# Optimization experiments

Measured on AMD Instinct MI355X. Metric: run time of the kernel, lower is better.

## Reference

```python
import jax, jax.numpy as jnp
import numpy as np

B, T, I, O, M = 64, 512, 256, 1024, 8
MS = O // M          # module_size
IM = I * M           # input_dim * num_modules


def setup_inputs() -> dict:
    key = jax.random.key(0)
    ks = jax.random.split(key, 6)
    s = 0.02
    return {
        "x": jax.random.normal(ks[0], (B, T, I), dtype=jnp.float32),
        "W_in": jax.random.normal(ks[1], (O, I), dtype=jnp.float32) * s,
        "b_in": jnp.zeros((O,), dtype=jnp.float32),
        "W_h": jax.random.normal(ks[2], (O, O), dtype=jnp.float32) * s,
        "W_ir": jax.random.normal(ks[3], (IM, I), dtype=jnp.float32) * s,
        "b_ir": jnp.zeros((IM,), dtype=jnp.float32),
        "W_hr": jax.random.normal(ks[4], (IM, IM), dtype=jnp.float32) * s,
        "module_periods": jnp.ones((M,), dtype=jnp.float32),
        "module_shifts": jnp.zeros((M,), dtype=jnp.float32),
    }


def reference(x, W_in, b_in, W_h, W_ir, b_ir, W_hr, module_periods, module_shifts):
    # x: [B, T, I]
    def step(carry, inp):
        h, x_pred = carry           # h: [B,O], x_pred: [B,IM]
        ti, xi = inp                # ti scalar float, xi: [B,I]
        acts = jnp.tanh(xi @ W_in.T + b_in + h @ W_h.T)            # [B,O]
        acts_rec = jnp.tanh(xi @ W_ir.T + b_ir + x_pred @ W_hr.T)  # [B,IM]
        m_xp = x_pred.reshape(B, M, I)
        # NOTE: nn.LogSoftmax() with no dim on a 3D tensor defaults to dim=0 (batch axis)
        surprisal = jax.nn.log_softmax(m_xp, axis=0) * xi[:, None, :]  # [B,M,I]
        mean_surprisal = surprisal.mean(-1)                            # [B,M]
        mp = mean_surprisal * module_periods                           # [B,M]
        gate = (jnp.sin(ti * mp + module_shifts) + 1.0) * 0.5          # [B,M]
        gate_full = jnp.repeat(gate, MS, axis=-1)                      # [B,O]
        y = (1.0 - gate_full) * acts + gate_full * h
        return (y, acts_rec), (y, mp)

    ts = jnp.arange(T, dtype=x.dtype)
    carry0 = (jnp.zeros((B, O), dtype=x.dtype), jnp.zeros((B, IM), dtype=x.dtype))
    (h_final, _), (ys, ps) = jax.lax.scan(step, carry0, (ts, jnp.swapaxes(x, 0, 1)))
    ys = jnp.swapaxes(ys, 0, 1)   # [B,T,O]
    ps = jnp.swapaxes(ps, 0, 1)   # [B,T,M]
    return ys, h_final, ps
```

## Files before the change

kernel.cpp:

```cpp
#include <hip/hip_runtime.h>
#include <hip/hip_fp16.h>

typedef _Float16 f16;
typedef f16 f16x8 __attribute__((ext_vector_type(8)));
typedef f16 f16x4 __attribute__((ext_vector_type(4)));
typedef float f32x4 __attribute__((ext_vector_type(4)));
typedef float f32x16 __attribute__((ext_vector_type(16)));

#define B_ 64
#define T_ 512
#define I_ 256
#define O_ 1024
#define M_ 8
#define IM_ 2048
#define NREC 64
#define NB 96
#define THREADS 256

#define OFF_X16 4096ull
#define SZ_X16  ((unsigned long long)T_ * B_ * I_ * 2)
#define OFF_XP3 (OFF_X16 + SZ_X16)
#define SZ_XP3  (3ull * B_ * IM_ * 2)
#define OFF_H2  (OFF_XP3 + SZ_XP3)

#define BAR_LEAF(i) ((i) * 16)
#define BAR_CENT    128
#define BAR_REPL(i) (192 + (i) * 16)

#define WAITV(N) asm volatile("s_waitcnt vmcnt(" #N ")" ::: "memory")
#define LGKM0    asm volatile("s_waitcnt lgkmcnt(0)" ::: "memory")
#define SCHEDB   __builtin_amdgcn_sched_barrier(0)
#define BARRIER  __builtin_amdgcn_s_barrier()

#define ISSUE_AX(BUF, P) asm volatile( \
    "global_load_dwordx4 %0, %8, off\n\t" \
    "global_load_dwordx4 %1, %8, off offset:32\n\t" \
    "global_load_dwordx4 %2, %8, off offset:64\n\t" \
    "global_load_dwordx4 %3, %8, off offset:96\n\t" \
    "global_load_dwordx4 %4, %8, off offset:128\n\t" \
    "global_load_dwordx4 %5, %8, off offset:160\n\t" \
    "global_load_dwordx4 %6, %8, off offset:192\n\t" \
    "global_load_dwordx4 %7, %8, off offset:224" \
    : "=&v"(abuf[BUF][0]), "=&v"(abuf[BUF][1]), "=&v"(abuf[BUF][2]), "=&v"(abuf[BUF][3]), \
      "=&v"(abuf[BUF][4]), "=&v"(abuf[BUF][5]), "=&v"(abuf[BUF][6]), "=&v"(abuf[BUF][7]) \
    : "v"(P) : "memory")

#define ISSUE_AS(BUF, P) asm volatile( \
    "global_load_dwordx4 %0, %8, off sc0 sc1\n\t" \
    "global_load_dwordx4 %1, %8, off offset:32 sc0 sc1\n\t" \
    "global_load_dwordx4 %2, %8, off offset:64 sc0 sc1\n\t" \
    "global_load_dwordx4 %3, %8, off offset:96 sc0 sc1\n\t" \
    "global_load_dwordx4 %4, %8, off offset:128 sc0 sc1\n\t" \
    "global_load_dwordx4 %5, %8, off offset:160 sc0 sc1\n\t" \
    "global_load_dwordx4 %6, %8, off offset:192 sc0 sc1\n\t" \
    "global_load_dwordx4 %7, %8, off offset:224 sc0 sc1" \
    : "=&v"(abuf[BUF][0]), "=&v"(abuf[BUF][1]), "=&v"(abuf[BUF][2]), "=&v"(abuf[BUF][3]), \
      "=&v"(abuf[BUF][4]), "=&v"(abuf[BUF][5]), "=&v"(abuf[BUF][6]), "=&v"(abuf[BUF][7]) \
    : "v"(P) : "memory")

#define ISSUE_STG8(P0,P1,P2,P3,P4,P5,P6,P7) asm volatile( \
    "global_load_dwordx4 %0, %8, off sc0 sc1\n\t" \
    "global_load_dwordx4 %1, %9, off sc0 sc1\n\t" \
    "global_load_dwordx4 %2, %10, off sc0 sc1\n\t" \
    "global_load_dwordx4 %3, %11, off sc0 sc1\n\t" \
    "global_load_dwordx4 %4, %12, off sc0 sc1\n\t" \
    "global_load_dwordx4 %5, %13, off sc0 sc1\n\t" \
    "global_load_dwordx4 %6, %14, off sc0 sc1\n\t" \
    "global_load_dwordx4 %7, %15, off sc0 sc1" \
    : "=&v"(sreg[0]), "=&v"(sreg[1]), "=&v"(sreg[2]), "=&v"(sreg[3]), \
      "=&v"(sreg[4]), "=&v"(sreg[5]), "=&v"(sreg[6]), "=&v"(sreg[7]) \
    : "v"(P0), "v"(P1), "v"(P2), "v"(P3), "v"(P4), "v"(P5), "v"(P6), "v"(P7) \
    : "memory")

#define GM_PRO(J) do { \
    const int c_ = c0 + (J); \
    if (c_ < 2) { const char* p_ = xrow + c_ * 256;  ISSUE_AX(J, p_); } \
    else        { const char* p_ = sprow + c_ * 256; ISSUE_AS(J, p_); } \
} while (0)

#define GM_ITR(I, WN, DOISS) do { \
    WAITV(WN); \
    _Pragma("unroll") \
    for (int kb = 0; kb < 8; ++kb) { \
        f16x8 bf = *(const f16x8*)(smem + addrB[kb] + (I) * 256); \
        if (kb & 1) acc1 = __builtin_amdgcn_mfma_f32_32x32x16_f16(abuf[(I) & 3][kb], bf, acc1, 0, 0, 0); \
        else        acc0 = __builtin_amdgcn_mfma_f32_32x32x16_f16(abuf[(I) & 3][kb], bf, acc0, 0, 0, 0); \
    } \
    SCHEDB; \
    if (DOISS) { const char* p_ = sprow + (c0 + (I) + 4) * 256; ISSUE_AS(((I) & 3), p_); } \
} while (0)

#define GM_ITA(I, WN, DOISS) do { \
    WAITV(WN); \
    _Pragma("unroll") \
    for (int kb = 0; kb < 8; ++kb) { \
        f16x8 bf = *(const f16x8*)(smem + addrB[kb] + (I) * 256); \
        if (kb & 1) acc1 = __builtin_amdgcn_mfma_f32_32x32x16_f16(abuf[(I) % 3][kb], bf, acc1, 0, 0, 0); \
        else        acc0 = __builtin_amdgcn_mfma_f32_32x32x16_f16(abuf[(I) % 3][kb], bf, acc0, 0, 0, 0); \
    } \
    SCHEDB; \
    if (DOISS) { const char* p_ = sprow + (c0 + (I) + 3) * 256; ISSUE_AS(((I) % 3), p_); } \
} while (0)

__device__ __forceinline__ void st_coh_h(f16* p, float vf) {
    union { f16 h; short s; } u; u.h = (f16)vf;
    asm volatile("global_store_short %0, %1, off sc0 sc1" :: "v"(p), "v"((int)u.s) : "memory");
}

__device__ __forceinline__ float fast_tanh(float x) {
    float e = __expf(2.f * x);
    return 1.f - 2.f / (e + 1.f);
}

__device__ __forceinline__ unsigned ld_rlx(unsigned* p) {
    return __hip_atomic_load(p, __ATOMIC_RELAXED, __HIP_MEMORY_SCOPE_AGENT);
}

__device__ __forceinline__ void arrive_all(unsigned* bar, int blk, int t) {
    unsigned old = __hip_atomic_fetch_add(&bar[BAR_LEAF(blk & 7)], 1u, __ATOMIC_RELAXED, __HIP_MEMORY_SCOPE_AGENT);
    if (old % 12u == 11u) {
        unsigned r = __hip_atomic_fetch_add(&bar[BAR_CENT], 1u, __ATOMIC_RELAXED, __HIP_MEMORY_SCOPE_AGENT);
        if ((r & 7u) == 7u) {
            unsigned v = (unsigned)(t + 1);
            #pragma unroll
            for (int i = 0; i < 8; ++i) {
                unsigned* rp = &bar[BAR_REPL(i)];
                asm volatile("global_store_dword %0, %1, off sc0 sc1" :: "v"(rp), "v"(v) : "memory");
            }
        }
    }
}

__global__ void init_kernel(const float* __restrict__ x, char* __restrict__ ws) {
    const int gid = blockIdx.x * THREADS + threadIdx.x;
    if (blockIdx.x == 0) {
        for (int i = threadIdx.x; i < 512; i += THREADS) ((unsigned*)ws)[i] = 0u;
    }
    f16* x16 = (f16*)(ws + OFF_X16);
    const int NQ = T_ * B_ * (I_ / 4);
    for (int q = gid; q < NQ; q += 256 * THREADS) {
        int t = q >> 12;
        int rem = q & 4095;
        int b = rem >> 6;
        int k4 = rem & 63;
        f32x4 v = *(const f32x4*)(x + ((size_t)b * T_ + t) * I_ + k4 * 4);
        f16x4 h;
        h[0] = (f16)v[0]; h[1] = (f16)v[1]; h[2] = (f16)v[2]; h[3] = (f16)v[3];
        *(f16x4*)(x16 + ((size_t)t * B_ + b) * I_ + k4 * 4) = h;
    }
    f16x8 z = {0, 0, 0, 0, 0, 0, 0, 0};
    f16* xp0 = (f16*)(ws + OFF_XP3);
    for (int e = gid * 8; e < B_ * IM_; e += 256 * THREADS * 8) *(f16x8*)(xp0 + e) = z;
    f16* h0 = (f16*)(ws + OFF_H2);
    for (int e = gid * 8; e < B_ * O_; e += 256 * THREADS * 8) *(f16x8*)(h0 + e) = z;
}

__global__ __launch_bounds__(THREADS, 1) void cwrnn_kernel(
    const float* __restrict__ x, const float* __restrict__ W_in, const float* __restrict__ b_in,
    const float* __restrict__ W_h, const float* __restrict__ W_ir, const float* __restrict__ b_ir,
    const float* __restrict__ W_hr, const float* __restrict__ periods, const float* __restrict__ shifts,
    float* __restrict__ out, char* __restrict__ ws)
{
    __shared__ __align__(16) char smem[157696];

    unsigned* bar = (unsigned*)ws;
    const int blk = blockIdx.x, tid = threadIdx.x;
    const int lane = tid & 63, w = tid >> 6;
    const int col = lane & 31, g = lane >> 5;
    const int pair = w >> 1;
    const int arow = ((w & 1) << 5) + col;

    float* ys = out;
    float* hfin = out + (size_t)B_ * T_ * O_;
    float* ps = hfin + (size_t)B_ * O_;

    unsigned* myrepl = &bar[BAR_REPL(blk & 7)];

    if (blk < NREC) {
        const int j0 = blk * 32;
        {
            const int j = tid >> 3;
            const float* ra = W_ir + (size_t)(j0 + j) * I_;
            const float* rb = W_hr + (size_t)(j0 + j) * IM_ - 256;
            for (int u = (tid & 7); u < 288; u += 8) {
                int k0 = u * 8;
                const float* s = (k0 < 256) ? (ra + k0) : (rb + k0);
                f32x4 lo = *(const f32x4*)s;
                f32x4 hi = *(const f32x4*)(s + 4);
                f16x8 v;
                #pragma unroll
                for (int e = 0; e < 4; ++e) { v[e] = (f16)lo[e]; v[e + 4] = (f16)hi[e]; }
                *(f16x8*)(smem + j * 4608 + ((u ^ (j & 15)) << 4)) = v;
            }
        }
        const float bir = b_ir[j0 + col];
        LGKM0; BARRIER;

        int addrB[8];
        const int c0 = pair * 9;
        #pragma unroll
        for (int kb = 0; kb < 8; ++kb)
            addrB[kb] = col * 4608 + ((((kb << 1) + g) ^ (col & 15)) << 4) + c0 * 256;

        const char* xrow0 = (const char*)(ws + OFF_X16) + (size_t)arow * 512 + g * 16;
        f16* const xpB = (f16*)(ws + OFF_XP3);

        for (int t = 0; t < T_ - 1; ++t) {
            if (tid == 0) {
                while ((int)ld_rlx(myrepl) < t) __builtin_amdgcn_s_sleep(2);
            }
            BARRIER;
            const int bi = t % 3;
            int bn = bi + 1; if (bn == 3) bn = 0;
            const f16* xpcur = xpB + (size_t)bi * B_ * IM_;
            f16* xpnxt = xpB + (size_t)bn * B_ * IM_;
            const char* sprow = (const char*)xpcur + (size_t)arow * 4096 + g * 16 - 512;
            const char* xrow = xrow0 + (size_t)t * 32768;

            f16x8 abuf[4][8];
            f32x16 acc0, acc1;
            #pragma unroll
            for (int r = 0; r < 16; ++r) { acc0[r] = 0.f; acc1[r] = 0.f; }

            GM_PRO(0); GM_PRO(1); GM_PRO(2); GM_PRO(3);
            GM_ITR(0, 24, 1); GM_ITR(1, 24, 1); GM_ITR(2, 24, 1); GM_ITR(3, 24, 1);
            GM_ITR(4, 24, 1); GM_ITR(5, 24, 0); GM_ITR(6, 16, 0); GM_ITR(7, 8, 0); GM_ITR(8, 0, 0);

            f32x16 accS;
            #pragma unroll
            for (int r = 0; r < 16; ++r) accS[r] = acc0[r] + acc1[r];
            if (w >= 2) {
                char* axp = smem + 147456 + (w - 2) * 5120 + lane * 80;
                #pragma unroll
                for (int q = 0; q < 4; ++q) {
                    f32x4 v = { accS[q * 4 + 0], accS[q * 4 + 1], accS[q * 4 + 2], accS[q * 4 + 3] };
                    *(f32x4*)(axp + q * 16) = v;
                }
            }
            LGKM0; BARRIER;
            if (w < 2) {
                const char* axp = smem + 147456 + w * 5120 + lane * 80;
                #pragma unroll
                for (int q = 0; q < 4; ++q) {
                    f32x4 v = *(const f32x4*)(axp + q * 16);
                    accS[q * 4 + 0] += v[0]; accS[q * 4 + 1] += v[1];
                    accS[q * 4 + 2] += v[2]; accS[q * 4 + 3] += v[3];
                }
                #pragma unroll
                for (int r = 0; r < 16; ++r) {
                    int row = (r & 3) + ((r >> 2) << 3) + (g << 2) + (w << 5);
                    st_coh_h(xpnxt + (size_t)row * IM_ + j0 + col, fast_tanh(accS[r] + bir));
                }
            }
            WAITV(0);
            BARRIER;
            if (tid == 0) arrive_all(bar, blk, t);
        }
    } else {
        const int a = blk - NREC;
        const int m = a >> 2;
        const int o0 = a * 32;
        {
            const int j = tid >> 3;
            const float* ra = W_in + (size_t)(o0 + j) * I_;
            const float* rb = W_h + (size_t)(o0 + j) * O_ - 256;
            for (int u = (tid & 7); u < 160; u += 8) {
                int k0 = u * 8;
                const float* s = (k0 < 256) ? (ra + k0) : (rb + k0);
                f32x4 lo = *(const f32x4*)s;
                f32x4 hi = *(const f32x4*)(s + 4);
                f16x8 v;
                #pragma unroll
                for (int e = 0; e < 4; ++e) { v[e] = (f16)lo[e]; v[e + 4] = (f16)hi[e]; }
                *(f16x8*)(smem + j * 2560 + ((u ^ (j & 15)) << 4)) = v;
            }
        }
        const float bin = b_in[o0 + col];
        const float per = periods[m], shf = shifts[m];
        LGKM0; BARRIER;

        int addrB[8];
        const int c0 = pair * 5;
        #pragma unroll
        for (int kb = 0; kb < 8; ++kb)
            addrB[kb] = col * 2560 + ((((kb << 1) + g) ^ (col & 15)) << 4) + c0 * 256;

        char* xp_raw = smem + 81920;
        float* lse_lds = (float*)(smem + 124928);
        float* part_lds = (float*)(smem + 125952);
        float* gate_lds = (float*)(smem + 126976);

        const char* xrow0 = (const char*)(ws + OFF_X16) + (size_t)arow * 512 + g * 16;
        const f16* xpB = (const f16*)(ws + OFF_XP3);
        f16* h2 = (f16*)(ws + OFF_H2);
        const int t5 = tid >> 5, cg = tid & 31;
        float hreg[16];
        #pragma unroll
        for (int r = 0; r < 16; ++r) hreg[r] = 0.f;

        for (int t = 0; t < T_; ++t) {
            if (tid == 0) {
                while ((int)ld_rlx(myrepl) < t) __builtin_amdgcn_s_sleep(2);
            }
            BARRIER;
            const int bi = t % 3;
            const f16* xpcur = xpB + (size_t)bi * B_ * IM_;
            const f16* hcur = h2 + (size_t)(t & 1) * B_ * O_;
            f16* hnxt = h2 + (size_t)((t + 1) & 1) * B_ * O_;

            f16x8 sreg[8];
            {
                const char* sb = (const char*)xpcur + (size_t)m * 512 + (size_t)cg * 16 + (size_t)t5 * 4096;
                ISSUE_STG8(sb, sb + 32768, sb + 2 * 32768, sb + 3 * 32768,
                           sb + 4 * 32768, sb + 5 * 32768, sb + 6 * 32768, sb + 7 * 32768);
            }

            const char* sprow = (const char*)hcur + (size_t)arow * 2048 + g * 16 - 512;
            const char* xrow = xrow0 + (size_t)t * 32768;
            f16x8 abuf[3][8];
            f32x16 acc0, acc1;
            #pragma unroll
            for (int r = 0; r < 16; ++r) { acc0[r] = 0.f; acc1[r] = 0.f; }

            GM_PRO(0); GM_PRO(1); GM_PRO(2);
            WAITV(16);
            {
                const int gsw = (cg ^ t5) << 4;
                #pragma unroll
                for (int k = 0; k < 8; ++k)
                    *(f16x8*)(xp_raw + (size_t)(t5 + (k << 3)) * 512 + gsw) = sreg[k];
            }
            #pragma unroll
            for (int kb = 0; kb < 8; ++kb) {
                f16x8 bf = *(const f16x8*)(smem + addrB[kb]);
                if (kb & 1) acc1 = __builtin_amdgcn_mfma_f32_32x32x16_f16(abuf[0][kb], bf, acc1, 0, 0, 0);
                else        acc0 = __builtin_amdgcn_mfma_f32_32x32x16_f16(abuf[0][kb], bf, acc0, 0, 0, 0);
            }
            SCHEDB;
            { const char* p_ = sprow + (c0 + 3) * 256; ISSUE_AS(0, p_); }
            GM_ITA(1, 16, 1); GM_ITA(2, 16, 0); GM_ITA(3, 8, 0); GM_ITA(4, 0, 0);

            f32x16 accS;
            #pragma unroll
            for (int r = 0; r < 16; ++r) accS[r] = acc0[r] + acc1[r];
            if (w >= 2) {
                char* axp = smem + 114688 + (w - 2) * 5120 + lane * 80;
                #pragma unroll
                for (int q = 0; q < 4; ++q) {
                    f32x4 v = { accS[q * 4 + 0], accS[q * 4 + 1], accS[q * 4 + 2], accS[q * 4 + 3] };
                    *(f32x4*)(axp + q * 16) = v;
                }
            }
            LGKM0; BARRIER;
            {
                int i = tid;
                int gq = i >> 3, r2 = (i & 7) * 2;
                float s = 0.f;
                #pragma unroll 8
                for (int b = 0; b < B_; ++b)
                    s += __expf((float)*(const f16*)(xp_raw + b * 512 + ((gq ^ (b & 7)) << 4) + r2));
                lse_lds[i] = __logf(s);
            }
            LGKM0; BARRIER;
            {
                int b = tid >> 2, q = tid & 3;
                const float* xr = x + ((size_t)b * T_ + t) * I_ + q * 64;
                float s = 0.f;
                #pragma unroll
                for (int k = 0; k < 8; ++k) {
                    f16x8 xp8 = *(const f16x8*)(xp_raw + (size_t)b * 512 + ((((q << 3) + k) ^ (b & 7)) << 4));
                    f32x4 xa = *(const f32x4*)(xr + k * 8);
                    f32x4 xb2 = *(const f32x4*)(xr + k * 8 + 4);
                    #pragma unroll
                    for (int jj = 0; jj < 4; ++jj)
                        s += ((float)xp8[jj] - lse_lds[(q << 6) + (k << 3) + jj]) * xa[jj];
                    #pragma unroll
                    for (int jj = 0; jj < 4; ++jj)
                        s += ((float)xp8[jj + 4] - lse_lds[(q << 6) + (k << 3) + 4 + jj]) * xb2[jj];
                }
                part_lds[tid] = s;
            }
            LGKM0; BARRIER;
            if (tid < B_) {
                float s = part_lds[tid * 4] + part_lds[tid * 4 + 1] + part_lds[tid * 4 + 2] + part_lds[tid * 4 + 3];
                float mp = (s * (1.f / 256.f)) * per;
                gate_lds[tid] = 0.5f * (sinf((float)t * mp + shf) + 1.f);
                if ((a & 3) == 0) ps[((size_t)tid * T_ + t) * M_ + m] = mp;
            }
            LGKM0; BARRIER;
            if (w < 2) {
                const char* axp = smem + 114688 + w * 5120 + lane * 80;
                #pragma unroll
                for (int q = 0; q < 4; ++q) {
                    f32x4 v = *(const f32x4*)(axp + q * 16);
                    accS[q * 4 + 0] += v[0]; accS[q * 4 + 1] += v[1];
                    accS[q * 4 + 2] += v[2]; accS[q * 4 + 3] += v[3];
                }
                #pragma unroll
                for (int r = 0; r < 16; ++r) {
                    int row = (r & 3) + ((r >> 2) << 3) + (g << 2) + (w << 5);
                    float gt = gate_lds[row];
                    float av = fast_tanh(accS[r] + bin);
                    float y = (1.f - gt) * av + gt * hreg[r];
                    hreg[r] = y;
                    st_coh_h(hnxt + (size_t)row * O_ + o0 + col, y);
                    ys[((size_t)row * T_ + t) * O_ + o0 + col] = y;
                    if (t == T_ - 1) hfin[(size_t)row * O_ + o0 + col] = y;
                }
            }
            WAITV(0);
            BARRIER;
            if (tid == 0) arrive_all(bar, blk, t);
        }
    }
}

extern "C" void kernel_launch(void* const* d_in, const int* in_sizes, int n_in,
                              void* d_out, int out_size, void* d_ws, size_t ws_size,
                              hipStream_t stream) {
    const float* x    = (const float*)d_in[0];
    const float* W_in = (const float*)d_in[1];
    const float* b_in = (const float*)d_in[2];
    const float* W_h  = (const float*)d_in[3];
    const float* W_ir = (const float*)d_in[4];
    const float* b_ir = (const float*)d_in[5];
    const float* W_hr = (const float*)d_in[6];
    const float* per  = (const float*)d_in[7];
    const float* shf  = (const float*)d_in[8];

    hipLaunchKernelGGL(init_kernel, dim3(256), dim3(THREADS), 0, stream,
                       x, (char*)d_ws);
    hipLaunchKernelGGL(cwrnn_kernel, dim3(NB), dim3(THREADS), 0, stream,
                       x, W_in, b_in, W_h, W_ir, b_ir, W_hr, per, shf,
                       (float*)d_out, (char*)d_ws);
}
```

Before: 6.467 ms.

## Split grid barrier into two groups and widen blocks to six waves

```diff
diff --git a/kernel.cpp b/kernel.cpp
--- a/kernel.cpp
+++ b/kernel.cpp
@@ -15,7 +15,7 @@
 #define IM_ 2048
 #define NREC 64
 #define NB 96
-#define THREADS 256
+#define THREADS 384
 
 #define OFF_X16 4096ull
 #define SZ_X16  ((unsigned long long)T_ * B_ * I_ * 2)
@@ -23,9 +23,20 @@
 #define SZ_XP3  (3ull * B_ * IM_ * 2)
 #define OFF_H2  (OFF_XP3 + SZ_XP3)
 
-#define BAR_LEAF(i) ((i) * 16)
-#define BAR_CENT    128
-#define BAR_REPL(i) (192 + (i) * 16)
+#define LEAFA(i) ((i) * 16)
+#define CENTA    128
+#define FLAGA(i) (192 + (i) * 16)
+#define LEAFB(i) (320 + (i) * 16)
+#define CENTB    448
+#define FLAGB(i) (512 + (i) * 16)
+
+#define CMB_REC 147456
+#define CMB_ACT 114688
+#define XPRAW   81920
+#define LSE_O   122880
+#define PART_O  123904
+#define GATE_O  124928
+#define SMEM_SZ 155648
 
 #define WAITV(N) asm volatile("s_waitcnt vmcnt(" #N ")" ::: "memory")
 #define LGKM0    asm volatile("s_waitcnt lgkmcnt(0)" ::: "memory")
@@ -58,7 +69,7 @@
       "=&v"(abuf[BUF][4]), "=&v"(abuf[BUF][5]), "=&v"(abuf[BUF][6]), "=&v"(abuf[BUF][7]) \
     : "v"(P) : "memory")
 
-#define ISSUE_STG8(P0,P1,P2,P3,P4,P5,P6,P7) asm volatile( \
+#define ISSUE_STGA(ARR, P0,P1,P2,P3,P4,P5,P6,P7) asm volatile( \
     "global_load_dwordx4 %0, %8, off sc0 sc1\n\t" \
     "global_load_dwordx4 %1, %9, off sc0 sc1\n\t" \
     "global_load_dwordx4 %2, %10, off sc0 sc1\n\t" \
@@ -67,30 +78,18 @@
     "global_load_dwordx4 %5, %13, off sc0 sc1\n\t" \
     "global_load_dwordx4 %6, %14, off sc0 sc1\n\t" \
     "global_load_dwordx4 %7, %15, off sc0 sc1" \
-    : "=&v"(sreg[0]), "=&v"(sreg[1]), "=&v"(sreg[2]), "=&v"(sreg[3]), \
-      "=&v"(sreg[4]), "=&v"(sreg[5]), "=&v"(sreg[6]), "=&v"(sreg[7]) \
+    : "=&v"((ARR)[0]), "=&v"((ARR)[1]), "=&v"((ARR)[2]), "=&v"((ARR)[3]), \
+      "=&v"((ARR)[4]), "=&v"((ARR)[5]), "=&v"((ARR)[6]), "=&v"((ARR)[7]) \
     : "v"(P0), "v"(P1), "v"(P2), "v"(P3), "v"(P4), "v"(P5), "v"(P6), "v"(P7) \
     : "memory")
 
 #define GM_PRO(J) do { \
-    const int c_ = c0 + (J); \
+    const int c_ = c0k + (J); \
     if (c_ < 2) { const char* p_ = xrow + c_ * 256;  ISSUE_AX(J, p_); } \
     else        { const char* p_ = sprow + c_ * 256; ISSUE_AS(J, p_); } \
 } while (0)
 
-#define GM_ITR(I, WN, DOISS) do { \
-    WAITV(WN); \
-    _Pragma("unroll") \
-    for (int kb = 0; kb < 8; ++kb) { \
-        f16x8 bf = *(const f16x8*)(smem + addrB[kb] + (I) * 256); \
-        if (kb & 1) acc1 = __builtin_amdgcn_mfma_f32_32x32x16_f16(abuf[(I) & 3][kb], bf, acc1, 0, 0, 0); \
-        else        acc0 = __builtin_amdgcn_mfma_f32_32x32x16_f16(abuf[(I) & 3][kb], bf, acc0, 0, 0, 0); \
-    } \
-    SCHEDB; \
-    if (DOISS) { const char* p_ = sprow + (c0 + (I) + 4) * 256; ISSUE_AS(((I) & 3), p_); } \
-} while (0)
-
-#define GM_ITA(I, WN, DOISS) do { \
+#define GM_IT(I, WN, DOISS) do { \
     WAITV(WN); \
     _Pragma("unroll") \
     for (int kb = 0; kb < 8; ++kb) { \
@@ -99,7 +98,7 @@
         else        acc0 = __builtin_amdgcn_mfma_f32_32x32x16_f16(abuf[(I) % 3][kb], bf, acc0, 0, 0, 0); \
     } \
     SCHEDB; \
-    if (DOISS) { const char* p_ = sprow + (c0 + (I) + 3) * 256; ISSUE_AS(((I) % 3), p_); } \
+    if (DOISS) { const char* p_ = sprow + (c0k + (I) + 3) * 256; ISSUE_AS(((I) % 3), p_); } \
 } while (0)
 
 __device__ __forceinline__ void st_coh_h(f16* p, float vf) {
@@ -116,29 +115,37 @@
     return __hip_atomic_load(p, __ATOMIC_RELAXED, __HIP_MEMORY_SCOPE_AGENT);
 }
 
-__device__ __forceinline__ void arrive_all(unsigned* bar, int blk, int t) {
-    unsigned old = __hip_atomic_fetch_add(&bar[BAR_LEAF(blk & 7)], 1u, __ATOMIC_RELAXED, __HIP_MEMORY_SCOPE_AGENT);
-    if (old % 12u == 11u) {
-        unsigned r = __hip_atomic_fetch_add(&bar[BAR_CENT], 1u, __ATOMIC_RELAXED, __HIP_MEMORY_SCOPE_AGENT);
-        if ((r & 7u) == 7u) {
-            unsigned v = (unsigned)(t + 1);
-            #pragma unroll
-            for (int i = 0; i < 8; ++i) {
-                unsigned* rp = &bar[BAR_REPL(i)];
-                asm volatile("global_store_dword %0, %1, off sc0 sc1" :: "v"(rp), "v"(v) : "memory");
-            }
-        }
+__device__ __forceinline__ void post_flags(unsigned* bar, int base, unsigned v) {
+    #pragma unroll
+    for (int i = 0; i < 8; ++i) {
+        unsigned* rp = &bar[base + i * 16];
+        asm volatile("global_store_dword %0, %1, off sc0 sc1" :: "v"(rp), "v"(v) : "memory");
     }
 }
 
+__device__ __forceinline__ void arriveA(unsigned* bar, int blk, int t) {
+    unsigned old = __hip_atomic_fetch_add(&bar[LEAFA(blk & 7)], 1u, __ATOMIC_RELAXED, __HIP_MEMORY_SCOPE_AGENT);
+    if ((old & 7u) == 7u) {
+        unsigned r = __hip_atomic_fetch_add(&bar[CENTA], 1u, __ATOMIC_RELAXED, __HIP_MEMORY_SCOPE_AGENT);
+        if ((r & 7u) == 7u) post_flags(bar, FLAGA(0), (unsigned)(t + 1));
+    }
+}
+__device__ __forceinline__ void arriveB(unsigned* bar, int a, int t) {
+    unsigned old = __hip_atomic_fetch_add(&bar[LEAFB(a & 7)], 1u, __ATOMIC_RELAXED, __HIP_MEMORY_SCOPE_AGENT);
+    if ((old & 3u) == 3u) {
+        unsigned r = __hip_atomic_fetch_add(&bar[CENTB], 1u, __ATOMIC_RELAXED, __HIP_MEMORY_SCOPE_AGENT);
+        if ((r & 7u) == 7u) post_flags(bar, FLAGB(0), (unsigned)(t + 1));
+    }
+}
+
 __global__ void init_kernel(const float* __restrict__ x, char* __restrict__ ws) {
-    const int gid = blockIdx.x * THREADS + threadIdx.x;
+    const int gid = blockIdx.x * 256 + threadIdx.x;
     if (blockIdx.x == 0) {
-        for (int i = threadIdx.x; i < 512; i += THREADS) ((unsigned*)ws)[i] = 0u;
+        for (int i = threadIdx.x; i < 1024; i += 256) ((unsigned*)ws)[i] = 0u;
     }
     f16* x16 = (f16*)(ws + OFF_X16);
     const int NQ = T_ * B_ * (I_ / 4);
-    for (int q = gid; q < NQ; q += 256 * THREADS) {
+    for (int q = gid; q < NQ; q += 256 * 256) {
         int t = q >> 12;
         int rem = q & 4095;
         int b = rem >> 6;
@@ -150,9 +157,9 @@
     }
     f16x8 z = {0, 0, 0, 0, 0, 0, 0, 0};
     f16* xp0 = (f16*)(ws + OFF_XP3);
-    for (int e = gid * 8; e < B_ * IM_; e += 256 * THREADS * 8) *(f16x8*)(xp0 + e) = z;
+    for (int e = gid * 8; e < B_ * IM_; e += 256 * 256 * 8) *(f16x8*)(xp0 + e) = z;
     f16* h0 = (f16*)(ws + OFF_H2);
-    for (int e = gid * 8; e < B_ * O_; e += 256 * THREADS * 8) *(f16x8*)(h0 + e) = z;
+    for (int e = gid * 8; e < B_ * O_; e += 256 * 256 * 8) *(f16x8*)(h0 + e) = z;
 }
 
 __global__ __launch_bounds__(THREADS, 1) void cwrnn_kernel(
@@ -161,28 +168,27 @@
     const float* __restrict__ W_hr, const float* __restrict__ periods, const float* __restrict__ shifts,
     float* __restrict__ out, char* __restrict__ ws)
 {
-    __shared__ __align__(16) char smem[157696];
+    __shared__ __align__(16) char smem[SMEM_SZ];
 
     unsigned* bar = (unsigned*)ws;
     const int blk = blockIdx.x, tid = threadIdx.x;
     const int lane = tid & 63, w = tid >> 6;
     const int col = lane & 31, g = lane >> 5;
-    const int pair = w >> 1;
-    const int arow = ((w & 1) << 5) + col;
+    const int rg = w & 1;
+    const int kg = w >> 1;
+    const int arow = (rg << 5) + col;
 
     float* ys = out;
     float* hfin = out + (size_t)B_ * T_ * O_;
     float* ps = hfin + (size_t)B_ * O_;
 
-    unsigned* myrepl = &bar[BAR_REPL(blk & 7)];
-
     if (blk < NREC) {
         const int j0 = blk * 32;
         {
-            const int j = tid >> 3;
+            const int j = tid & 31;
             const float* ra = W_ir + (size_t)(j0 + j) * I_;
             const float* rb = W_hr + (size_t)(j0 + j) * IM_ - 256;
-            for (int u = (tid & 7); u < 288; u += 8) {
+            for (int u = (tid >> 5); u < 288; u += 12) {
                 int k0 = u * 8;
                 const float* s = (k0 < 256) ? (ra + k0) : (rb + k0);
                 f32x4 lo = *(const f32x4*)s;
@@ -197,17 +203,24 @@
         LGKM0; BARRIER;
 
         int addrB[8];
-        const int c0 = pair * 9;
+        const int c0k = kg * 6;
         #pragma unroll
         for (int kb = 0; kb < 8; ++kb)
-            addrB[kb] = col * 4608 + ((((kb << 1) + g) ^ (col & 15)) << 4) + c0 * 256;
+            addrB[kb] = col * 4608 + ((((kb << 1) + g) ^ (col & 15)) << 4) + c0k * 256;
 
         const char* xrow0 = (const char*)(ws + OFF_X16) + (size_t)arow * 512 + g * 16;
         f16* const xpB = (f16*)(ws + OFF_XP3);
+        unsigned* fA = &bar[FLAGA(blk & 7)];
+        unsigned* fB = &bar[FLAGB(blk & 7)];
 
         for (int t = 0; t < T_ - 1; ++t) {
             if (tid == 0) {
-                while ((int)ld_rlx(myrepl) < t) __builtin_amdgcn_s_sleep(2);
+                while (1) {
+                    int fa = (int)ld_rlx(fA);
+                    int fb = (int)ld_rlx(fB);
+                    if (fa >= t && fb >= t - 2) break;
+                    __builtin_amdgcn_s_sleep(2);
+                }
             }
             BARRIER;
             const int bi = t % 3;
@@ -217,54 +230,74 @@
             const char* sprow = (const char*)xpcur + (size_t)arow * 4096 + g * 16 - 512;
             const char* xrow = xrow0 + (size_t)t * 32768;
 
-            f16x8 abuf[4][8];
+            f16x8 abuf[3][8];
             f32x16 acc0, acc1;
             #pragma unroll
             for (int r = 0; r < 16; ++r) { acc0[r] = 0.f; acc1[r] = 0.f; }
 
-            GM_PRO(0); GM_PRO(1); GM_PRO(2); GM_PRO(3);
-            GM_ITR(0, 24, 1); GM_ITR(1, 24, 1); GM_ITR(2, 24, 1); GM_ITR(3, 24, 1);
-            GM_ITR(4, 24, 1); GM_ITR(5, 24, 0); GM_ITR(6, 16, 0); GM_ITR(7, 8, 0); GM_ITR(8, 0, 0);
+            GM_PRO(0); GM_PRO(1); GM_PRO(2);
+            GM_IT(0, 16, 1); GM_IT(1, 16, 1); GM_IT(2, 16, 1);
+            GM_IT(3, 16, 0); GM_IT(4, 8, 0); GM_IT(5, 0, 0);
 
             f32x16 accS;
             #pragma unroll
             for (int r = 0; r < 16; ++r) accS[r] = acc0[r] + acc1[r];
-            if (w >= 2) {
-                char* axp = smem + 147456 + (w - 2) * 5120 + lane * 80;
-                #pragma unroll
-                for (int q = 0; q < 4; ++q) {
-                    f32x4 v = { accS[q * 4 + 0], accS[q * 4 + 1], accS[q * 4 + 2], accS[q * 4 + 3] };
-                    *(f32x4*)(axp + q * 16) = v;
-                }
-            }
-            LGKM0; BARRIER;
-            if (w < 2) {
-                const char* axp = smem + 147456 + w * 5120 + lane * 80;
-                #pragma unroll
-                for (int q = 0; q < 4; ++q) {
-                    f32x4 v = *(const f32x4*)(axp + q * 16);
-                    accS[q * 4 + 0] += v[0]; accS[q * 4 + 1] += v[1];
-                    accS[q * 4 + 2] += v[2]; accS[q * 4 + 3] += v[3];
+
+            if (kg == 1) {
+                char* cb = smem + CMB_REC + rg * 4096 + lane * 16;
+                #pragma unroll
+                for (int q = 0; q < 4; ++q) {
+                    f32x4 v = { accS[q*4+0], accS[q*4+1], accS[q*4+2], accS[q*4+3] };
+                    *(f32x4*)(cb + q * 1024) = v;
+                }
+            }
+            LGKM0; BARRIER;
+            if (kg == 0) {
+                const char* cb = smem + CMB_REC + rg * 4096 + lane * 16;
+                #pragma unroll
+                for (int q = 0; q < 4; ++q) {
+                    f32x4 v = *(const f32x4*)(cb + q * 1024);
+                    accS[q*4+0] += v[0]; accS[q*4+1] += v[1];
+                    accS[q*4+2] += v[2]; accS[q*4+3] += v[3];
+                }
+            }
+            LGKM0; BARRIER;
+            if (kg == 2) {
+                char* cb = smem + CMB_REC + rg * 4096 + lane * 16;
+                #pragma unroll
+                for (int q = 0; q < 4; ++q) {
+                    f32x4 v = { accS[q*4+0], accS[q*4+1], accS[q*4+2], accS[q*4+3] };
+                    *(f32x4*)(cb + q * 1024) = v;
+                }
+            }
+            LGKM0; BARRIER;
+            if (kg == 0) {
+                const char* cb = smem + CMB_REC + rg * 4096 + lane * 16;
+                #pragma unroll
+                for (int q = 0; q < 4; ++q) {
+                    f32x4 v = *(const f32x4*)(cb + q * 1024);
+                    accS[q*4+0] += v[0]; accS[q*4+1] += v[1];
+                    accS[q*4+2] += v[2]; accS[q*4+3] += v[3];
                 }
                 #pragma unroll
                 for (int r = 0; r < 16; ++r) {
-                    int row = (r & 3) + ((r >> 2) << 3) + (g << 2) + (w << 5);
+                    int row = (r & 3) + ((r >> 2) << 3) + (g << 2) + (rg << 5);
                     st_coh_h(xpnxt + (size_t)row * IM_ + j0 + col, fast_tanh(accS[r] + bir));
                 }
             }
             WAITV(0);
             BARRIER;
-            if (tid == 0) arrive_all(bar, blk, t);
+            if (tid == 0) arriveA(bar, blk, t);
         }
     } else {
         const int a = blk - NREC;
         const int m = a >> 2;
         const int o0 = a * 32;
         {
-            const int j = tid >> 3;
+            const int j = tid & 31;
             const float* ra = W_in + (size_t)(o0 + j) * I_;
             const float* rb = W_h + (size_t)(o0 + j) * O_ - 256;
-            for (int u = (tid & 7); u < 160; u += 8) {
+            for (int u = (tid >> 5); u < 160; u += 12) {
                 int k0 = u * 8;
                 const float* s = (k0 < 256) ? (ra + k0) : (rb + k0);
                 f32x4 lo = *(const f32x4*)s;
@@ -280,27 +313,33 @@
         LGKM0; BARRIER;
 
         int addrB[8];
-        const int c0 = pair * 5;
+        const int c0k = kg * 4;
         #pragma unroll
         for (int kb = 0; kb < 8; ++kb)
-            addrB[kb] = col * 2560 + ((((kb << 1) + g) ^ (col & 15)) << 4) + c0 * 256;
-
-        char* xp_raw = smem + 81920;
-        float* lse_lds = (float*)(smem + 124928);
-        float* part_lds = (float*)(smem + 125952);
-        float* gate_lds = (float*)(smem + 126976);
+            addrB[kb] = col * 2560 + ((((kb << 1) + g) ^ (col & 15)) << 4) + c0k * 256;
+
+        char* xp_raw = smem + XPRAW;
+        float* lse_lds = (float*)(smem + LSE_O);
+        float* part_lds = (float*)(smem + PART_O);
+        float* gate_lds = (float*)(smem + GATE_O);
 
         const char* xrow0 = (const char*)(ws + OFF_X16) + (size_t)arow * 512 + g * 16;
         const f16* xpB = (const f16*)(ws + OFF_XP3);
         f16* h2 = (f16*)(ws + OFF_H2);
-        const int t5 = tid >> 5, cg = tid & 31;
+        unsigned* fA = &bar[FLAGA(a & 7)];
+        unsigned* fB = &bar[FLAGB(a & 7)];
         float hreg[16];
         #pragma unroll
         for (int r = 0; r < 16; ++r) hreg[r] = 0.f;
 
         for (int t = 0; t < T_; ++t) {
             if (tid == 0) {
-                while ((int)ld_rlx(myrepl) < t) __builtin_amdgcn_s_sleep(2);
+                while (1) {
+                    int fa = (int)ld_rlx(fA);
+                    int fb = (int)ld_rlx(fB);
+                    if (fa >= t && fb >= t) break;
+                    __builtin_amdgcn_s_sleep(2);
+                }
             }
             BARRIER;
             const int bi = t % 3;
@@ -308,51 +347,69 @@
             const f16* hcur = h2 + (size_t)(t & 1) * B_ * O_;
             f16* hnxt = h2 + (size_t)((t + 1) & 1) * B_ * O_;
 
-            f16x8 sreg[8];
-            {
-                const char* sb = (const char*)xpcur + (size_t)m * 512 + (size_t)cg * 16 + (size_t)t5 * 4096;
-                ISSUE_STG8(sb, sb + 32768, sb + 2 * 32768, sb + 3 * 32768,
-                           sb + 4 * 32768, sb + 5 * 32768, sb + 6 * 32768, sb + 7 * 32768);
-            }
-
             const char* sprow = (const char*)hcur + (size_t)arow * 2048 + g * 16 - 512;
             const char* xrow = xrow0 + (size_t)t * 32768;
             f16x8 abuf[3][8];
+            f16x8 sreg[8], sreg2[8];
             f32x16 acc0, acc1;
             #pragma unroll
             for (int r = 0; r < 16; ++r) { acc0[r] = 0.f; acc1[r] = 0.f; }
 
-            GM_PRO(0); GM_PRO(1); GM_PRO(2);
-            WAITV(16);
-            {
-                const int gsw = (cg ^ t5) << 4;
-                #pragma unroll
-                for (int k = 0; k < 8; ++k)
-                    *(f16x8*)(xp_raw + (size_t)(t5 + (k << 3)) * 512 + gsw) = sreg[k];
-            }
-            #pragma unroll
-            for (int kb = 0; kb < 8; ++kb) {
-                f16x8 bf = *(const f16x8*)(smem + addrB[kb]);
-                if (kb & 1) acc1 = __builtin_amdgcn_mfma_f32_32x32x16_f16(abuf[0][kb], bf, acc1, 0, 0, 0);
-                else        acc0 = __builtin_amdgcn_mfma_f32_32x32x16_f16(abuf[0][kb], bf, acc0, 0, 0, 0);
-            }
-            SCHEDB;
-            { const char* p_ = sprow + (c0 + 3) * 256; ISSUE_AS(0, p_); }
-            GM_ITA(1, 16, 1); GM_ITA(2, 16, 0); GM_ITA(3, 8, 0); GM_ITA(4, 0, 0);
+            if (kg < 2) {
+                GM_PRO(0); GM_PRO(1); GM_PRO(2);
+                GM_IT(0, 16, 1); GM_IT(1, 16, 0); GM_IT(2, 8, 0); GM_IT(3, 0, 0);
+            } else {
+                { const char* p_ = sprow + 8 * 256; ISSUE_AS(0, p_); }
+                { const char* p_ = sprow + 9 * 256; ISSUE_AS(1, p_); }
+                const int l = tid - 256;
+                const int t5a = l >> 5, cga = l & 31;
+                const int t5b = (l + 128) >> 5, cgb = l & 31;
+                const char* sa = (const char*)xpcur + (size_t)m * 512 + cga * 16 + (size_t)t5a * 4096;
+                const char* sb = (const char*)xpcur + (size_t)m * 512 + cgb * 16 + (size_t)t5b * 4096;
+                ISSUE_STGA(sreg,  sa, sa + 32768, sa + 2*32768, sa + 3*32768,
+                                  sa + 4*32768, sa + 5*32768, sa + 6*32768, sa + 7*32768);
+                ISSUE_STGA(sreg2, sb, sb + 32768, sb + 2*32768, sb + 3*32768,
+                                  sb + 4*32768, sb + 5*32768, sb + 6*32768, sb + 7*32768);
+                WAITV(24);
+                #pragma unroll
+                for (int kb = 0; kb < 8; ++kb) {
+                    f16x8 bf = *(const f16x8*)(smem + addrB[kb]);
+                    if (kb & 1) acc1 = __builtin_amdgcn_mfma_f32_32x32x16_f16(abuf[0][kb], bf, acc1, 0, 0, 0);
+                    else        acc0 = __builtin_amdgcn_mfma_f32_32x32x16_f16(abuf[0][kb], bf, acc0, 0, 0, 0);
+                }
+                WAITV(16);
+                #pragma unroll
+                for (int kb = 0; kb < 8; ++kb) {
+                    f16x8 bf = *(const f16x8*)(smem + addrB[kb] + 256);
+                    if (kb & 1) acc1 = __builtin_amdgcn_mfma_f32_32x32x16_f16(abuf[1][kb], bf, acc1, 0, 0, 0);
+                    else        acc0 = __builtin_amdgcn_mfma_f32_32x32x16_f16(abuf[1][kb], bf, acc0, 0, 0, 0);
+                }
+                WAITV(0); SCHEDB;
+                {
+                    const int gswa = (cga ^ t5a) << 4;
+                    const int gswb = (cgb ^ t5b) << 4;
+                    #pragma unroll
+                    for (int k = 0; k < 8; ++k) {
+                        *(f16x8*)(xp_raw + (size_t)(t5a + (k << 3)) * 512 + gswa) = sreg[k];
+                        *(f16x8*)(xp_raw + (size_t)(t5b + (k << 3)) * 512 + gswb) = sreg2[k];
+                    }
+                }
+            }
 
             f32x16 accS;
             #pragma unroll
             for (int r = 0; r < 16; ++r) accS[r] = acc0[r] + acc1[r];
-            if (w >= 2) {
-                char* axp = smem + 114688 + (w - 2) * 5120 + lane * 80;
-                #pragma unroll
-                for (int q = 0; q < 4; ++q) {
-                    f32x4 v = { accS[q * 4 + 0], accS[q * 4 + 1], accS[q * 4 + 2], accS[q * 4 + 3] };
-                    *(f32x4*)(axp + q * 16) = v;
-                }
-            }
-            LGKM0; BARRIER;
-            {
+
+            if (kg == 1) {
+                char* cb = smem + CMB_ACT + rg * 4096 + lane * 16;
+                #pragma unroll
+                for (int q = 0; q < 4; ++q) {
+                    f32x4 v = { accS[q*4+0], accS[q*4+1], accS[q*4+2], accS[q*4+3] };
+                    *(f32x4*)(cb + q * 1024) = v;
+                }
+            }
+            LGKM0; BARRIER;
+            if (tid < 256) {
                 int i = tid;
                 int gq = i >> 3, r2 = (i & 7) * 2;
                 float s = 0.f;
@@ -361,8 +418,25 @@
                     s += __expf((float)*(const f16*)(xp_raw + b * 512 + ((gq ^ (b & 7)) << 4) + r2));
                 lse_lds[i] = __logf(s);
             }
-            LGKM0; BARRIER;
-            {
+            if (kg == 0) {
+                const char* cb = smem + CMB_ACT + rg * 4096 + lane * 16;
+                #pragma unroll
+                for (int q = 0; q < 4; ++q) {
+                    f32x4 v = *(const f32x4*)(cb + q * 1024);
+                    accS[q*4+0] += v[0]; accS[q*4+1] += v[1];
+                    accS[q*4+2] += v[2]; accS[q*4+3] += v[3];
+                }
+            }
+            LGKM0; BARRIER;
+            if (kg == 2) {
+                char* cb = smem + CMB_ACT + rg * 4096 + lane * 16;
+                #pragma unroll
+                for (int q = 0; q < 4; ++q) {
+                    f32x4 v = { accS[q*4+0], accS[q*4+1], accS[q*4+2], accS[q*4+3] };
+                    *(f32x4*)(cb + q * 1024) = v;
+                }
+            }
+            if (tid < 256) {
                 int b = tid >> 2, q = tid & 3;
                 const float* xr = x + ((size_t)b * T_ + t) * I_ + q * 64;
                 float s = 0.f;
@@ -387,18 +461,20 @@
                 gate_lds[tid] = 0.5f * (sinf((float)t * mp + shf) + 1.f);
                 if ((a & 3) == 0) ps[((size_t)tid * T_ + t) * M_ + m] = mp;
             }
-            LGKM0; BARRIER;
-            if (w < 2) {
-                const char* axp = smem + 114688 + w * 5120 + lane * 80;
-                #pragma unroll
-                for (int q = 0; q < 4; ++q) {
-                    f32x4 v = *(const f32x4*)(axp + q * 16);
-                    accS[q * 4 + 0] += v[0]; accS[q * 4 + 1] += v[1];
-                    accS[q * 4 + 2] += v[2]; accS[q * 4 + 3] += v[3];
-                }
+            if (kg == 0) {
+                const char* cb = smem + CMB_ACT + rg * 4096 + lane * 16;
+                #pragma unroll
+                for (int q = 0; q < 4; ++q) {
+                    f32x4 v = *(const f32x4*)(cb + q * 1024);
+                    accS[q*4+0] += v[0]; accS[q*4+1] += v[1];
+                    accS[q*4+2] += v[2]; accS[q*4+3] += v[3];
+                }
+            }
+            LGKM0; BARRIER;
+            if (kg == 0) {
                 #pragma unroll
                 for (int r = 0; r < 16; ++r) {
-                    int row = (r & 3) + ((r >> 2) << 3) + (g << 2) + (w << 5);
+                    int row = (r & 3) + ((r >> 2) << 3) + (g << 2) + (rg << 5);
                     float gt = gate_lds[row];
                     float av = fast_tanh(accS[r] + bin);
                     float y = (1.f - gt) * av + gt * hreg[r];
@@ -410,7 +486,7 @@
             }
             WAITV(0);
             BARRIER;
-            if (tid == 0) arrive_all(bar, blk, t);
+            if (tid == 0) arriveB(bar, a, t);
         }
     }
 }
@@ -428,7 +504,7 @@
     const float* per  = (const float*)d_in[7];
     const float* shf  = (const float*)d_in[8];
 
-    hipLaunchKernelGGL(init_kernel, dim3(256), dim3(THREADS), 0, stream,
+    hipLaunchKernelGGL(init_kernel, dim3(256), dim3(256), 0, stream,
                        x, (char*)d_ws);
     hipLaunchKernelGGL(cwrnn_kernel, dim3(NB), dim3(THREADS), 0, stream,
                        x, W_in, b_in, W_h, W_ir, b_ir, W_hr, per, shf,
```

Result: slower. 11.43 ms (+76.8%).
